# Performance work log

Measured on AMD Instinct MI355X. Metric: run time of the kernel, lower is better.

Reference implementation:

```python
import jax, jax.numpy as jnp
import numpy as np

D_MODEL = 768
NUM_HEADS = 12
HEAD_DIM = D_MODEL // NUM_HEADS
LN_EPS = 1e-5
MASK_NEG = -1000000.0


def setup_inputs() -> dict:
    key = jax.random.key(0)
    ks = jax.random.split(key, 10)
    B, L, S = 2, 2048, 2048
    s = 1.0 / np.sqrt(D_MODEL)
    return {
        "q": jax.random.normal(ks[0], (B, L, D_MODEL), jnp.float32),
        "k": jax.random.normal(ks[1], (B, S, D_MODEL), jnp.float32),
        "v": jax.random.normal(ks[2], (B, S, D_MODEL), jnp.float32),
        "attention_mask": jnp.ones((B, S), jnp.int32),
        "Wq": jax.random.normal(ks[3], (D_MODEL, D_MODEL), jnp.float32) * s,
        "Wk": jax.random.normal(ks[4], (D_MODEL, D_MODEL), jnp.float32) * s,
        "Wv": jax.random.normal(ks[5], (D_MODEL, D_MODEL), jnp.float32) * s,
        "W": jax.random.normal(ks[6], (D_MODEL, D_MODEL), jnp.float32) * s,
        "b": jnp.zeros((D_MODEL,), jnp.float32),
        "gamma": jnp.ones((D_MODEL,), jnp.float32),
        "beta": jnp.zeros((D_MODEL,), jnp.float32),
    }


def reference(q, k, v, attention_mask, Wq, Wk, Wv, W, b, gamma, beta):
    B, L, D = q.shape
    S = k.shape[1]
    H, hd = NUM_HEADS, HEAD_DIM
    # projections (torch Linear: x @ W^T), split heads -> (B,H,L,hd)
    Q = (q @ Wq.T).reshape(B, L, H, hd).transpose(0, 2, 1, 3)
    K = (k @ Wk.T).reshape(B, S, H, hd).transpose(0, 2, 1, 3)
    V = (v @ Wv.T).reshape(B, S, H, hd).transpose(0, 2, 1, 3)
    # scores (B,H,L,S) with additive key-padding mask
    scores = jnp.einsum("bhld,bhsd->bhls", Q, K) / np.sqrt(hd)
    mask_score = (1.0 - attention_mask.astype(q.dtype))[:, None, None, :] * MASK_NEG
    att = jax.nn.softmax(scores + mask_score, axis=-1)  # dropout p=0 (eval)
    # attend, merge heads, output projection (with bias)
    O = jnp.einsum("bhls,bhsd->bhld", att, V).transpose(0, 2, 1, 3).reshape(B, L, D)
    O = O @ W.T + b  # state dropout p=0 (eval)
    # residual + LayerNorm
    x = q + O
    mu = jnp.mean(x, axis=-1, keepdims=True)
    var = jnp.mean(jnp.square(x - mu), axis=-1, keepdims=True)
    return (x - mu) * jax.lax.rsqrt(var + LN_EPS) * gamma + beta
```

## Files before the change

kernel.cpp:

```cpp
#include <hip/hip_runtime.h>
#include <hip/hip_bf16.h>
#include <math.h>


typedef unsigned short u16;
typedef unsigned int   u32;
typedef __bf16 bf16x8 __attribute__((ext_vector_type(8)));
typedef float  f32x4  __attribute__((ext_vector_type(4)));

#define DM   768
#define MR   4096
#define WSZ  589824

#define LOG2E 1.44269504089f
#define SM_C  15.0f
#define K1    (0.125f * LOG2E)

__device__ inline u16 bfbits(float f) {
    union { __bf16 b; u16 u; } x; x.b = (__bf16)f; return x.u;
}

__device__ inline uint4 cvt8(const float* src) {
    const float4* p = reinterpret_cast<const float4*>(src);
    float4 a = p[0], b = p[1];
    union { __bf16 h[8]; uint4 v; } u;
    u.h[0] = (__bf16)a.x; u.h[1] = (__bf16)a.y; u.h[2] = (__bf16)a.z; u.h[3] = (__bf16)a.w;
    u.h[4] = (__bf16)b.x; u.h[5] = (__bf16)b.y; u.h[6] = (__bf16)b.z; u.h[7] = (__bf16)b.w;
    return u.v;
}

__device__ inline uint4 cvt8v(float4 a, float4 b) {
    union { __bf16 h[8]; uint4 v; } u;
    u.h[0] = (__bf16)a.x; u.h[1] = (__bf16)a.y; u.h[2] = (__bf16)a.z; u.h[3] = (__bf16)a.w;
    u.h[4] = (__bf16)b.x; u.h[5] = (__bf16)b.y; u.h[6] = (__bf16)b.z; u.h[7] = (__bf16)b.w;
    return u.v;
}

__global__ __launch_bounds__(256) void wcvt(
    const float* __restrict__ w0, const float* __restrict__ w1,
    const float* __restrict__ w2, const float* __restrict__ w3,
    u16* __restrict__ dst)
{
    const float* src = (blockIdx.y == 0) ? w0 : (blockIdx.y == 1) ? w1
                     : (blockIdx.y == 2) ? w2 : w3;
    size_t idx = ((size_t)blockIdx.x * 256 + threadIdx.x) * 8;
    *reinterpret_cast<uint4*>(&dst[(size_t)blockIdx.y * WSZ + idx]) = cvt8(&src[idx]);
}

__global__ __launch_bounds__(256, 2) void gemm_qkv(
    const float* __restrict__ xq, const float* __restrict__ xk, const float* __restrict__ xv,
    const u16* __restrict__ Wb4,
    u16* __restrict__ oq, u16* __restrict__ ok, u16* __restrict__ ov)
{
    const int mode = blockIdx.z;
    const float* X = (mode == 0) ? xq : (mode == 1) ? xk : xv;
    const u16* Wb  = Wb4 + (size_t)mode * WSZ;
    u16* out       = (mode == 0) ? oq : (mode == 1) ? ok : ov;

    __shared__ __attribute__((aligned(16))) u16 As[2][64][72];
    __shared__ __attribute__((aligned(16))) u16 Bs[64][72];

    const int tid  = threadIdx.x;
    const int lane = tid & 63;
    const int w    = tid >> 6;
    const int wm   = (w >> 1) * 32;
    const int wn   = (w & 1) * 32;
    const int quad = lane >> 4;
    const int l16  = lane & 15;
    const int tm   = blockIdx.x * 64;
    const int tn   = blockIdx.y * 64;

    const int row0 = tid >> 3,         col0 = (tid & 7) * 8;
    const int row1 = (tid + 256) >> 3, col1 = ((tid + 256) & 7) * 8;

    const float* a0p = &X[(size_t)(tm + row0) * 768 + col0];
    const float* a1p = &X[(size_t)(tm + row1) * 768 + col1];
    const u16*   b0p = &Wb[(size_t)(tn + row0) * 768 + col0];
    const u16*   b1p = &Wb[(size_t)(tn + row1) * 768 + col1];

    f32x4 acc[2][2] = {};

    *reinterpret_cast<uint4*>(&As[0][row0][col0]) = cvt8(a0p);
    *reinterpret_cast<uint4*>(&As[0][row1][col1]) = cvt8(a1p);
    uint4 bt0 = *reinterpret_cast<const uint4*>(b0p);
    uint4 bt1 = *reinterpret_cast<const uint4*>(b1p);

    for (int kt = 0; kt < 12; kt++) {
        const int cur = kt & 1;
        if (kt) __syncthreads();
        *reinterpret_cast<uint4*>(&Bs[row0][col0]) = bt0;
        *reinterpret_cast<uint4*>(&Bs[row1][col1]) = bt1;
        __syncthreads();

        float4 af0a, af0b, af1a, af1b;
        if (kt < 11) {
            const int ko = (kt + 1) * 64;
            af0a = *reinterpret_cast<const float4*>(a0p + ko);
            af0b = *reinterpret_cast<const float4*>(a0p + ko + 4);
            af1a = *reinterpret_cast<const float4*>(a1p + ko);
            af1b = *reinterpret_cast<const float4*>(a1p + ko + 4);
            bt0  = *reinterpret_cast<const uint4*>(b0p + ko);
            bt1  = *reinterpret_cast<const uint4*>(b1p + ko);
        }

        #pragma unroll
        for (int kk = 0; kk < 2; kk++) {
            bf16x8 a0 = *reinterpret_cast<const bf16x8*>(&As[cur][wm + l16     ][kk*32 + quad*8]);
            bf16x8 a1 = *reinterpret_cast<const bf16x8*>(&As[cur][wm + 16 + l16][kk*32 + quad*8]);
            bf16x8 b0 = *reinterpret_cast<const bf16x8*>(&Bs[wn + l16     ][kk*32 + quad*8]);
            bf16x8 b1 = *reinterpret_cast<const bf16x8*>(&Bs[wn + 16 + l16][kk*32 + quad*8]);
            acc[0][0] = __builtin_amdgcn_mfma_f32_16x16x32_bf16(a0, b0, acc[0][0], 0, 0, 0);
            acc[0][1] = __builtin_amdgcn_mfma_f32_16x16x32_bf16(a0, b1, acc[0][1], 0, 0, 0);
            acc[1][0] = __builtin_amdgcn_mfma_f32_16x16x32_bf16(a1, b0, acc[1][0], 0, 0, 0);
            acc[1][1] = __builtin_amdgcn_mfma_f32_16x16x32_bf16(a1, b1, acc[1][1], 0, 0, 0);
        }

        if (kt < 11) {
            const int nxt = cur ^ 1;
            *reinterpret_cast<uint4*>(&As[nxt][row0][col0]) = cvt8v(af0a, af0b);
            *reinterpret_cast<uint4*>(&As[nxt][row1][col1]) = cvt8v(af1a, af1b);
        }
    }

    #pragma unroll
    for (int i = 0; i < 2; i++)
        #pragma unroll
        for (int j = 0; j < 2; j++)
            #pragma unroll
            for (int r = 0; r < 4; r++) {
                int gm = tm + wm + i * 16 + quad * 4 + r;
                int gn = tn + wn + j * 16 + l16;
                int b = gm >> 11, l = gm & 2047;
                int h = gn >> 6,  d = gn & 63;
                u16 bv = bfbits(acc[i][j][r]);
                if (mode == 2)
                    out[((size_t)(b * 12 + h) * 64 + d) * 2048 + l] = bv;
                else
                    out[((size_t)(b * 12 + h) * 2048 + l) * 64 + d] = bv;
            }
}

__global__ __launch_bounds__(256, 2) void gemm_out(
    const u16* __restrict__ Oa, const u16* __restrict__ Wb,
    const float* __restrict__ bias, const float* __restrict__ resid,
    float* __restrict__ Xb)
{
    __shared__ __attribute__((aligned(16))) u16 As[2][64][72];
    __shared__ __attribute__((aligned(16))) u16 Bs[64][72];

    const int tid  = threadIdx.x;
    const int lane = tid & 63;
    const int w    = tid >> 6;
    const int wm   = (w >> 1) * 32;
    const int wn   = (w & 1) * 32;
    const int quad = lane >> 4;
    const int l16  = lane & 15;
    const int tm   = blockIdx.x * 64;
    const int tn   = blockIdx.y * 64;

    const int row0 = tid >> 3,         col0 = (tid & 7) * 8;
    const int row1 = (tid + 256) >> 3, col1 = ((tid + 256) & 7) * 8;

    const u16* a0p = &Oa[(size_t)(tm + row0) * 768 + col0];
    const u16* a1p = &Oa[(size_t)(tm + row1) * 768 + col1];
    const u16* b0p = &Wb[(size_t)(tn + row0) * 768 + col0];
    const u16* b1p = &Wb[(size_t)(tn + row1) * 768 + col1];

    f32x4 acc[2][2] = {};

    *reinterpret_cast<uint4*>(&As[0][row0][col0]) = *reinterpret_cast<const uint4*>(a0p);
    *reinterpret_cast<uint4*>(&As[0][row1][col1]) = *reinterpret_cast<const uint4*>(a1p);
    uint4 bt0 = *reinterpret_cast<const uint4*>(b0p);
    uint4 bt1 = *reinterpret_cast<const uint4*>(b1p);

    for (int kt = 0; kt < 12; kt++) {
        const int cur = kt & 1;
        if (kt) __syncthreads();
        *reinterpret_cast<uint4*>(&Bs[row0][col0]) = bt0;
        *reinterpret_cast<uint4*>(&Bs[row1][col1]) = bt1;
        __syncthreads();

        uint4 at0, at1;
        if (kt < 11) {
            const int ko = (kt + 1) * 64;
            at0 = *reinterpret_cast<const uint4*>(a0p + ko);
            at1 = *reinterpret_cast<const uint4*>(a1p + ko);
            bt0 = *reinterpret_cast<const uint4*>(b0p + ko);
            bt1 = *reinterpret_cast<const uint4*>(b1p + ko);
        }

        #pragma unroll
        for (int kk = 0; kk < 2; kk++) {
            bf16x8 a0 = *reinterpret_cast<const bf16x8*>(&As[cur][wm + l16     ][kk*32 + quad*8]);
            bf16x8 a1 = *reinterpret_cast<const bf16x8*>(&As[cur][wm + 16 + l16][kk*32 + quad*8]);
            bf16x8 b0 = *reinterpret_cast<const bf16x8*>(&Bs[wn + l16     ][kk*32 + quad*8]);
            bf16x8 b1 = *reinterpret_cast<const bf16x8*>(&Bs[wn + 16 + l16][kk*32 + quad*8]);
            acc[0][0] = __builtin_amdgcn_mfma_f32_16x16x32_bf16(a0, b0, acc[0][0], 0, 0, 0);
            acc[0][1] = __builtin_amdgcn_mfma_f32_16x16x32_bf16(a0, b1, acc[0][1], 0, 0, 0);
            acc[1][0] = __builtin_amdgcn_mfma_f32_16x16x32_bf16(a1, b0, acc[1][0], 0, 0, 0);
            acc[1][1] = __builtin_amdgcn_mfma_f32_16x16x32_bf16(a1, b1, acc[1][1], 0, 0, 0);
        }

        if (kt < 11) {
            const int nxt = cur ^ 1;
            *reinterpret_cast<uint4*>(&As[nxt][row0][col0]) = at0;
            *reinterpret_cast<uint4*>(&As[nxt][row1][col1]) = at1;
        }
    }

    #pragma unroll
    for (int i = 0; i < 2; i++)
        #pragma unroll
        for (int j = 0; j < 2; j++)
            #pragma unroll
            for (int r = 0; r < 4; r++) {
                int gm = tm + wm + i * 16 + quad * 4 + r;
                int gn = tn + wn + j * 16 + l16;
                Xb[(size_t)gm * 768 + gn] = acc[i][j][r] + bias[gn] + resid[(size_t)gm * 768 + gn];
            }
}

__global__ __launch_bounds__(256, 3) void attn(
    const u16* __restrict__ Qp, const u16* __restrict__ Kp, const u16* __restrict__ Vt,
    const int* __restrict__ amask, u16* __restrict__ Oatt)
{
    __shared__ __attribute__((aligned(16))) unsigned char smem[4 * 64 * 40 * 2 + 2048 * 4];
    u16 (*Ps)[64][40] = reinterpret_cast<u16(*)[64][40]>(smem);
    float* maskC = reinterpret_cast<float*>(smem + 20480);
    float (*Obuf)[68] = reinterpret_cast<float(*)[68]>(smem);

    const int tid  = threadIdx.x;
    const int lane = tid & 63;
    const int w    = tid >> 6;
    const int quad = lane >> 4;
    const int l16  = lane & 15;
    const int qt = blockIdx.x;
    const int h  = blockIdx.y;
    const int b  = blockIdx.z;

    #pragma unroll
    for (int i = 0; i < 8; i++) {
        int s = tid + i * 256;
        maskC[s] = amask[b * 2048 + s] ? (-SM_C * LOG2E) : -2.0e6f;
    }
    __syncthreads();

    const u16* Qbase = Qp + ((size_t)(b * 12 + h) * 2048 + qt * 64) * 64;
    const u16* Kb2   = Kp + (size_t)(b * 12 + h) * 2048 * 64 + (size_t)w * 32 * 64;
    const u16* Vb2   = Vt + (size_t)(b * 12 + h) * 64 * 2048 + (size_t)w * 32;

    bf16x8 qfrag[4][2];
    #pragma unroll
    for (int qb = 0; qb < 4; qb++)
        #pragma unroll
        for (int kk = 0; kk < 2; kk++)
            qfrag[qb][kk] = *reinterpret_cast<const bf16x8*>(
                &Qbase[(qb * 16 + l16) * 64 + kk * 32 + quad * 8]);

    bf16x8 onesf = {};
    if (l16 == 0) {
        #pragma unroll
        for (int i = 0; i < 8; i++) onesf[i] = (__bf16)1.0f;
    }

    f32x4 oacc[4][4] = {};
    f32x4 sacc[4]    = {};

    bf16x8 kf[2][2], vf[4];
    #pragma unroll
    for (int ct = 0; ct < 2; ct++)
        #pragma unroll
        for (int kk = 0; kk < 2; kk++)
            kf[ct][kk] = *reinterpret_cast<const bf16x8*>(
                &Kb2[(size_t)(ct * 16 + l16) * 64 + kk * 32 + quad * 8]);
    #pragma unroll
    for (int cd = 0; cd < 4; cd++)
        vf[cd] = *reinterpret_cast<const bf16x8*>(
            &Vb2[(size_t)(cd * 16 + l16) * 2048 + quad * 8]);

    for (int st = 0; st < 16; st++) {
        const int stn = (st + 1) & 15;

        #pragma unroll
        for (int ct = 0; ct < 2; ct++) {
            f32x4 sv[4];
            #pragma unroll
            for (int qb = 0; qb < 4; qb++) {
                f32x4 s = {};
                s = __builtin_amdgcn_mfma_f32_16x16x32_bf16(kf[ct][0], qfrag[qb][0], s, 0, 0, 0);
                s = __builtin_amdgcn_mfma_f32_16x16x32_bf16(kf[ct][1], qfrag[qb][1], s, 0, 0, 0);
                sv[qb] = s;
            }
            #pragma unroll
            for (int kk = 0; kk < 2; kk++)
                kf[ct][kk] = *reinterpret_cast<const bf16x8*>(
                    &Kb2[(size_t)(stn * 128 + ct * 16 + l16) * 64 + kk * 32 + quad * 8]);

            f32x4 cc = *reinterpret_cast<const f32x4*>(
                &maskC[st * 128 + w * 32 + ct * 16 + quad * 4]);
            #pragma unroll
            for (int qb = 0; qb < 4; qb++) {
                union { u16 h[4]; uint2 v2; } pk;
                #pragma unroll
                for (int r = 0; r < 4; r++)
                    pk.h[r] = bfbits(__builtin_amdgcn_exp2f(__builtin_fmaf(sv[qb][r], K1, cc[r])));
                *reinterpret_cast<uint2*>(&Ps[w][qb * 16 + l16][ct * 16 + quad * 4]) = pk.v2;
            }
        }

        bf16x8 pf[4];
        #pragma unroll
        for (int qb = 0; qb < 4; qb++)
            pf[qb] = *reinterpret_cast<const bf16x8*>(&Ps[w][qb * 16 + l16][quad * 8]);
        #pragma unroll
        for (int qb = 0; qb < 4; qb++)
            sacc[qb] = __builtin_amdgcn_mfma_f32_16x16x32_bf16(pf[qb], onesf, sacc[qb], 0, 0, 0);
        #pragma unroll
        for (int qb = 0; qb < 4; qb++)
            #pragma unroll
            for (int cd = 0; cd < 4; cd++)
                oacc[qb][cd] = __builtin_amdgcn_mfma_f32_16x16x32_bf16(pf[qb], vf[cd], oacc[qb][cd], 0, 0, 0);

        #pragma unroll
        for (int cd = 0; cd < 4; cd++)
            vf[cd] = *reinterpret_cast<const bf16x8*>(
                &Vb2[(size_t)(cd * 16 + l16) * 2048 + stn * 128 + quad * 8]);
    }

    __syncthreads();
    for (int wv = 0; wv < 4; wv++) {
        if (w == wv) {
            #pragma unroll
            for (int qb = 0; qb < 4; qb++) {
                #pragma unroll
                for (int cd = 0; cd < 4; cd++)
                    #pragma unroll
                    for (int r = 0; r < 4; r++) {
                        float* cell = &Obuf[qb * 16 + quad * 4 + r][cd * 16 + l16];
                        if (wv == 0) *cell = oacc[qb][cd][r];
                        else         *cell += oacc[qb][cd][r];
                    }
                if (l16 == 0) {
                    #pragma unroll
                    for (int r = 0; r < 4; r++) {
                        float* cell = &Obuf[qb * 16 + quad * 4 + r][64];
                        if (wv == 0) *cell = sacc[qb][r];
                        else         *cell += sacc[qb][r];
                    }
                }
            }
        }
        __syncthreads();
    }

    #pragma unroll
    for (int g = 0; g < 4; g++) {
        int unit = tid + g * 256;
        int row = unit >> 4;
        int c4  = (unit & 15) * 4;
        float rinv = 1.0f / Obuf[row][64];
        union { u16 h[4]; uint2 v; } o;
        #pragma unroll
        for (int j = 0; j < 4; j++)
            o.h[j] = bfbits(Obuf[row][c4 + j] * rinv);
        *reinterpret_cast<uint2*>(
            &Oatt[(size_t)(b * 2048 + qt * 64 + row) * 768 + h * 64 + c4]) = o.v;
    }
}

__global__ __launch_bounds__(256) void ln_kernel(
    float* __restrict__ X, const float* __restrict__ gamma,
    const float* __restrict__ beta)
{
    const int tid  = threadIdx.x;
    const int w    = tid >> 6;
    const int lane = tid & 63;
    const int row  = blockIdx.x * 4 + w;
    float* xr = X + (size_t)row * 768;

    float4 v[3];
    float s = 0.f, s2 = 0.f;
    #pragma unroll
    for (int i = 0; i < 3; i++) {
        v[i] = *reinterpret_cast<const float4*>(&xr[i * 256 + lane * 4]);
        s  += v[i].x + v[i].y + v[i].z + v[i].w;
        s2 += v[i].x * v[i].x + v[i].y * v[i].y + v[i].z * v[i].z + v[i].w * v[i].w;
    }
    #pragma unroll
    for (int off = 32; off >= 1; off >>= 1) {
        s  += __shfl_xor(s,  off, 64);
        s2 += __shfl_xor(s2, off, 64);
    }
    float mu  = s * (1.0f / 768.0f);
    float var = s2 * (1.0f / 768.0f) - mu * mu;
    float rstd = rsqrtf(var + 1e-5f);
    #pragma unroll
    for (int i = 0; i < 3; i++) {
        int c = i * 256 + lane * 4;
        float4 g  = *reinterpret_cast<const float4*>(&gamma[c]);
        float4 bt = *reinterpret_cast<const float4*>(&beta[c]);
        float4 o;
        o.x = (v[i].x - mu) * rstd * g.x + bt.x;
        o.y = (v[i].y - mu) * rstd * g.y + bt.y;
        o.z = (v[i].z - mu) * rstd * g.z + bt.z;
        o.w = (v[i].w - mu) * rstd * g.w + bt.w;
        *reinterpret_cast<float4*>(&xr[c]) = o;
    }
}

extern "C" void kernel_launch(void* const* d_in, const int* in_sizes, int n_in,
                              void* d_out, int out_size, void* d_ws, size_t ws_size,
                              hipStream_t stream)
{
    const float* q   = (const float*)d_in[0];
    const float* k   = (const float*)d_in[1];
    const float* v   = (const float*)d_in[2];
    const int*   am  = (const int*)d_in[3];
    const float* Wq  = (const float*)d_in[4];
    const float* Wk  = (const float*)d_in[5];
    const float* Wv  = (const float*)d_in[6];
    const float* W   = (const float*)d_in[7];
    const float* bb  = (const float*)d_in[8];
    const float* gam = (const float*)d_in[9];
    const float* bet = (const float*)d_in[10];

    u16* Wb4 = (u16*)d_ws;
    u16* Qp  = Wb4 + (size_t)4 * WSZ;
    u16* Kp  = Qp + (size_t)MR * DM;
    u16* Vt  = Kp + (size_t)MR * DM;
    u16* Oa  = Vt + (size_t)MR * DM;
    float* Xb = (float*)d_out;

    wcvt<<<dim3(288, 4), 256, 0, stream>>>(Wq, Wk, Wv, W, Wb4);
    gemm_qkv<<<dim3(64, 12, 3), 256, 0, stream>>>(q, k, v, Wb4, Qp, Kp, Vt);
    attn<<<dim3(32, 12, 2), 256, 0, stream>>>(Qp, Kp, Vt, am, Oa);
    gemm_out<<<dim3(64, 12), 256, 0, stream>>>(Oa, Wb4 + (size_t)3 * WSZ, bb, q, Xb);
    ln_kernel<<<1024, 256, 0, stream>>>(Xb, gam, bet);
}
```

Before: 214.9 us.

## Fuse weight bf16 conversion into GEMMs and split attention queries across 8 waves

Removes the separate weight-conversion kernel and has the QKV and output GEMMs load fp32 weights and convert them to bf16 while staging into shared memory. This saves one launch and the bf16 weight round-trip, but each GEMM block now reads twice as many weight bytes and converts the same weight tiles repeatedly. The attention kernel goes from 256 to 512 threads: 8 waves arranged as 4 key slices by 2 query halves, each holding half the accumulators. This lowers per-wave register use to raise occupancy, at the cost of every wave reading its full K/V slice, so K/V loads per block double.

```diff
diff --git a/kernel.cpp b/kernel.cpp
--- a/kernel.cpp
+++ b/kernel.cpp
@@ -10,7 +10,6 @@
 
 #define DM   768
 #define MR   4096
-#define WSZ  589824
 
 #define LOG2E 1.44269504089f
 #define SM_C  15.0f
@@ -36,26 +35,15 @@
     return u.v;
 }
 
-__global__ __launch_bounds__(256) void wcvt(
-    const float* __restrict__ w0, const float* __restrict__ w1,
-    const float* __restrict__ w2, const float* __restrict__ w3,
-    u16* __restrict__ dst)
-{
-    const float* src = (blockIdx.y == 0) ? w0 : (blockIdx.y == 1) ? w1
-                     : (blockIdx.y == 2) ? w2 : w3;
-    size_t idx = ((size_t)blockIdx.x * 256 + threadIdx.x) * 8;
-    *reinterpret_cast<uint4*>(&dst[(size_t)blockIdx.y * WSZ + idx]) = cvt8(&src[idx]);
-}
-
 __global__ __launch_bounds__(256, 2) void gemm_qkv(
     const float* __restrict__ xq, const float* __restrict__ xk, const float* __restrict__ xv,
-    const u16* __restrict__ Wb4,
+    const float* __restrict__ Wq, const float* __restrict__ Wk, const float* __restrict__ Wv,
     u16* __restrict__ oq, u16* __restrict__ ok, u16* __restrict__ ov)
 {
     const int mode = blockIdx.z;
-    const float* X = (mode == 0) ? xq : (mode == 1) ? xk : xv;
-    const u16* Wb  = Wb4 + (size_t)mode * WSZ;
-    u16* out       = (mode == 0) ? oq : (mode == 1) ? ok : ov;
+    const float* X  = (mode == 0) ? xq : (mode == 1) ? xk : xv;
+    const float* Wf = (mode == 0) ? Wq : (mode == 1) ? Wk : Wv;
+    u16* out        = (mode == 0) ? oq : (mode == 1) ? ok : ov;
 
     __shared__ __attribute__((aligned(16))) u16 As[2][64][72];
     __shared__ __attribute__((aligned(16))) u16 Bs[64][72];
@@ -75,21 +63,23 @@
 
     const float* a0p = &X[(size_t)(tm + row0) * 768 + col0];
     const float* a1p = &X[(size_t)(tm + row1) * 768 + col1];
-    const u16*   b0p = &Wb[(size_t)(tn + row0) * 768 + col0];
-    const u16*   b1p = &Wb[(size_t)(tn + row1) * 768 + col1];
+    const float* b0p = &Wf[(size_t)(tn + row0) * 768 + col0];
+    const float* b1p = &Wf[(size_t)(tn + row1) * 768 + col1];
 
     f32x4 acc[2][2] = {};
 
     *reinterpret_cast<uint4*>(&As[0][row0][col0]) = cvt8(a0p);
     *reinterpret_cast<uint4*>(&As[0][row1][col1]) = cvt8(a1p);
-    uint4 bt0 = *reinterpret_cast<const uint4*>(b0p);
-    uint4 bt1 = *reinterpret_cast<const uint4*>(b1p);
+    float4 bf0a = *reinterpret_cast<const float4*>(b0p);
+    float4 bf0b = *reinterpret_cast<const float4*>(b0p + 4);
+    float4 bf1a = *reinterpret_cast<const float4*>(b1p);
+    float4 bf1b = *reinterpret_cast<const float4*>(b1p + 4);
 
     for (int kt = 0; kt < 12; kt++) {
         const int cur = kt & 1;
         if (kt) __syncthreads();
-        *reinterpret_cast<uint4*>(&Bs[row0][col0]) = bt0;
-        *reinterpret_cast<uint4*>(&Bs[row1][col1]) = bt1;
+        *reinterpret_cast<uint4*>(&Bs[row0][col0]) = cvt8v(bf0a, bf0b);
+        *reinterpret_cast<uint4*>(&Bs[row1][col1]) = cvt8v(bf1a, bf1b);
         __syncthreads();
 
         float4 af0a, af0b, af1a, af1b;
@@ -99,8 +89,10 @@
             af0b = *reinterpret_cast<const float4*>(a0p + ko + 4);
             af1a = *reinterpret_cast<const float4*>(a1p + ko);
             af1b = *reinterpret_cast<const float4*>(a1p + ko + 4);
-            bt0  = *reinterpret_cast<const uint4*>(b0p + ko);
-            bt1  = *reinterpret_cast<const uint4*>(b1p + ko);
+            bf0a = *reinterpret_cast<const float4*>(b0p + ko);
+            bf0b = *reinterpret_cast<const float4*>(b0p + ko + 4);
+            bf1a = *reinterpret_cast<const float4*>(b1p + ko);
+            bf1b = *reinterpret_cast<const float4*>(b1p + ko + 4);
         }
 
         #pragma unroll
@@ -141,7 +133,7 @@
 }
 
 __global__ __launch_bounds__(256, 2) void gemm_out(
-    const u16* __restrict__ Oa, const u16* __restrict__ Wb,
+    const u16* __restrict__ Oa, const float* __restrict__ Wf,
     const float* __restrict__ bias, const float* __restrict__ resid,
     float* __restrict__ Xb)
 {
@@ -161,23 +153,25 @@
     const int row0 = tid >> 3,         col0 = (tid & 7) * 8;
     const int row1 = (tid + 256) >> 3, col1 = ((tid + 256) & 7) * 8;
 
-    const u16* a0p = &Oa[(size_t)(tm + row0) * 768 + col0];
-    const u16* a1p = &Oa[(size_t)(tm + row1) * 768 + col1];
-    const u16* b0p = &Wb[(size_t)(tn + row0) * 768 + col0];
-    const u16* b1p = &Wb[(size_t)(tn + row1) * 768 + col1];
+    const u16*   a0p = &Oa[(size_t)(tm + row0) * 768 + col0];
+    const u16*   a1p = &Oa[(size_t)(tm + row1) * 768 + col1];
+    const float* b0p = &Wf[(size_t)(tn + row0) * 768 + col0];
+    const float* b1p = &Wf[(size_t)(tn + row1) * 768 + col1];
 
     f32x4 acc[2][2] = {};
 
     *reinterpret_cast<uint4*>(&As[0][row0][col0]) = *reinterpret_cast<const uint4*>(a0p);
     *reinterpret_cast<uint4*>(&As[0][row1][col1]) = *reinterpret_cast<const uint4*>(a1p);
-    uint4 bt0 = *reinterpret_cast<const uint4*>(b0p);
-    uint4 bt1 = *reinterpret_cast<const uint4*>(b1p);
+    float4 bf0a = *reinterpret_cast<const float4*>(b0p);
+    float4 bf0b = *reinterpret_cast<const float4*>(b0p + 4);
+    float4 bf1a = *reinterpret_cast<const float4*>(b1p);
+    float4 bf1b = *reinterpret_cast<const float4*>(b1p + 4);
 
     for (int kt = 0; kt < 12; kt++) {
         const int cur = kt & 1;
         if (kt) __syncthreads();
-        *reinterpret_cast<uint4*>(&Bs[row0][col0]) = bt0;
-        *reinterpret_cast<uint4*>(&Bs[row1][col1]) = bt1;
+        *reinterpret_cast<uint4*>(&Bs[row0][col0]) = cvt8v(bf0a, bf0b);
+        *reinterpret_cast<uint4*>(&Bs[row1][col1]) = cvt8v(bf1a, bf1b);
         __syncthreads();
 
         uint4 at0, at1;
@@ -185,8 +179,10 @@
             const int ko = (kt + 1) * 64;
             at0 = *reinterpret_cast<const uint4*>(a0p + ko);
             at1 = *reinterpret_cast<const uint4*>(a1p + ko);
-            bt0 = *reinterpret_cast<const uint4*>(b0p + ko);
-            bt1 = *reinterpret_cast<const uint4*>(b1p + ko);
+            bf0a = *reinterpret_cast<const float4*>(b0p + ko);
+            bf0b = *reinterpret_cast<const float4*>(b0p + ko + 4);
+            bf1a = *reinterpret_cast<const float4*>(b1p + ko);
+            bf1b = *reinterpret_cast<const float4*>(b1p + ko + 4);
         }
 
         #pragma unroll
@@ -220,7 +216,7 @@
             }
 }
 
-__global__ __launch_bounds__(256, 3) void attn(
+__global__ __launch_bounds__(512, 4) void attn(
     const u16* __restrict__ Qp, const u16* __restrict__ Kp, const u16* __restrict__ Vt,
     const int* __restrict__ amask, u16* __restrict__ Oatt)
 {
@@ -232,6 +228,8 @@
     const int tid  = threadIdx.x;
     const int lane = tid & 63;
     const int w    = tid >> 6;
+    const int wk   = w & 3;
+    const int wq   = w >> 2;
     const int quad = lane >> 4;
     const int l16  = lane & 15;
     const int qt = blockIdx.x;
@@ -239,23 +237,23 @@
     const int b  = blockIdx.z;
 
     #pragma unroll
-    for (int i = 0; i < 8; i++) {
-        int s = tid + i * 256;
+    for (int i = 0; i < 4; i++) {
+        int s = tid + i * 512;
         maskC[s] = amask[b * 2048 + s] ? (-SM_C * LOG2E) : -2.0e6f;
     }
     __syncthreads();
 
     const u16* Qbase = Qp + ((size_t)(b * 12 + h) * 2048 + qt * 64) * 64;
-    const u16* Kb2   = Kp + (size_t)(b * 12 + h) * 2048 * 64 + (size_t)w * 32 * 64;
-    const u16* Vb2   = Vt + (size_t)(b * 12 + h) * 64 * 2048 + (size_t)w * 32;
-
-    bf16x8 qfrag[4][2];
-    #pragma unroll
-    for (int qb = 0; qb < 4; qb++)
+    const u16* Kb2   = Kp + (size_t)(b * 12 + h) * 2048 * 64 + (size_t)wk * 32 * 64;
+    const u16* Vb2   = Vt + (size_t)(b * 12 + h) * 64 * 2048 + (size_t)wk * 32;
+
+    bf16x8 qfrag[2][2];
+    #pragma unroll
+    for (int q = 0; q < 2; q++)
         #pragma unroll
         for (int kk = 0; kk < 2; kk++)
-            qfrag[qb][kk] = *reinterpret_cast<const bf16x8*>(
-                &Qbase[(qb * 16 + l16) * 64 + kk * 32 + quad * 8]);
+            qfrag[q][kk] = *reinterpret_cast<const bf16x8*>(
+                &Qbase[((wq * 2 + q) * 16 + l16) * 64 + kk * 32 + quad * 8]);
 
     bf16x8 onesf = {};
     if (l16 == 0) {
@@ -263,8 +261,8 @@
         for (int i = 0; i < 8; i++) onesf[i] = (__bf16)1.0f;
     }
 
-    f32x4 oacc[4][4] = {};
-    f32x4 sacc[4]    = {};
+    f32x4 oacc[2][4] = {};
+    f32x4 sacc[2]    = {};
 
     bf16x8 kf[2][2], vf[4];
     #pragma unroll
@@ -283,13 +281,13 @@
 
         #pragma unroll
         for (int ct = 0; ct < 2; ct++) {
-            f32x4 sv[4];
-            #pragma unroll
-            for (int qb = 0; qb < 4; qb++) {
+            f32x4 sv[2];
+            #pragma unroll
+            for (int q = 0; q < 2; q++) {
                 f32x4 s = {};
-                s = __builtin_amdgcn_mfma_f32_16x16x32_bf16(kf[ct][0], qfrag[qb][0], s, 0, 0, 0);
-                s = __builtin_amdgcn_mfma_f32_16x16x32_bf16(kf[ct][1], qfrag[qb][1], s, 0, 0, 0);
-                sv[qb] = s;
+                s = __builtin_amdgcn_mfma_f32_16x16x32_bf16(kf[ct][0], qfrag[q][0], s, 0, 0, 0);
+                s = __builtin_amdgcn_mfma_f32_16x16x32_bf16(kf[ct][1], qfrag[q][1], s, 0, 0, 0);
+                sv[q] = s;
             }
             #pragma unroll
             for (int kk = 0; kk < 2; kk++)
@@ -297,29 +295,31 @@
                     &Kb2[(size_t)(stn * 128 + ct * 16 + l16) * 64 + kk * 32 + quad * 8]);
 
             f32x4 cc = *reinterpret_cast<const f32x4*>(
-                &maskC[st * 128 + w * 32 + ct * 16 + quad * 4]);
-            #pragma unroll
-            for (int qb = 0; qb < 4; qb++) {
+                &maskC[st * 128 + wk * 32 + ct * 16 + quad * 4]);
+            #pragma unroll
+            for (int q = 0; q < 2; q++) {
                 union { u16 h[4]; uint2 v2; } pk;
                 #pragma unroll
                 for (int r = 0; r < 4; r++)
-                    pk.h[r] = bfbits(__builtin_amdgcn_exp2f(__builtin_fmaf(sv[qb][r], K1, cc[r])));
-                *reinterpret_cast<uint2*>(&Ps[w][qb * 16 + l16][ct * 16 + quad * 4]) = pk.v2;
+                    pk.h[r] = bfbits(__builtin_amdgcn_exp2f(__builtin_fmaf(sv[q][r], K1, cc[r])));
+                *reinterpret_cast<uint2*>(
+                    &Ps[wk][(wq * 2 + q) * 16 + l16][ct * 16 + quad * 4]) = pk.v2;
             }
         }
 
-        bf16x8 pf[4];
-        #pragma unroll
-        for (int qb = 0; qb < 4; qb++)
-            pf[qb] = *reinterpret_cast<const bf16x8*>(&Ps[w][qb * 16 + l16][quad * 8]);
-        #pragma unroll
-        for (int qb = 0; qb < 4; qb++)
-            sacc[qb] = __builtin_amdgcn_mfma_f32_16x16x32_bf16(pf[qb], onesf, sacc[qb], 0, 0, 0);
-        #pragma unroll
-        for (int qb = 0; qb < 4; qb++)
+        bf16x8 pf[2];
+        #pragma unroll
+        for (int q = 0; q < 2; q++)
+            pf[q] = *reinterpret_cast<const bf16x8*>(
+                &Ps[wk][(wq * 2 + q) * 16 + l16][quad * 8]);
+        #pragma unroll
+        for (int q = 0; q < 2; q++)
+            sacc[q] = __builtin_amdgcn_mfma_f32_16x16x32_bf16(pf[q], onesf, sacc[q], 0, 0, 0);
+        #pragma unroll
+        for (int q = 0; q < 2; q++)
             #pragma unroll
             for (int cd = 0; cd < 4; cd++)
-                oacc[qb][cd] = __builtin_amdgcn_mfma_f32_16x16x32_bf16(pf[qb], vf[cd], oacc[qb][cd], 0, 0, 0);
+                oacc[q][cd] = __builtin_amdgcn_mfma_f32_16x16x32_bf16(pf[q], vf[cd], oacc[q][cd], 0, 0, 0);
 
         #pragma unroll
         for (int cd = 0; cd < 4; cd++)
@@ -329,23 +329,24 @@
 
     __syncthreads();
     for (int wv = 0; wv < 4; wv++) {
-        if (w == wv) {
-            #pragma unroll
-            for (int qb = 0; qb < 4; qb++) {
+        if (wk == wv) {
+            #pragma unroll
+            for (int q = 0; q < 2; q++) {
+                const int rowb = (wq * 2 + q) * 16;
                 #pragma unroll
                 for (int cd = 0; cd < 4; cd++)
                     #pragma unroll
                     for (int r = 0; r < 4; r++) {
-                        float* cell = &Obuf[qb * 16 + quad * 4 + r][cd * 16 + l16];
-                        if (wv == 0) *cell = oacc[qb][cd][r];
-                        else         *cell += oacc[qb][cd][r];
+                        float* cell = &Obuf[rowb + quad * 4 + r][cd * 16 + l16];
+                        if (wv == 0) *cell = oacc[q][cd][r];
+                        else         *cell += oacc[q][cd][r];
                     }
                 if (l16 == 0) {
                     #pragma unroll
                     for (int r = 0; r < 4; r++) {
-                        float* cell = &Obuf[qb * 16 + quad * 4 + r][64];
-                        if (wv == 0) *cell = sacc[qb][r];
-                        else         *cell += sacc[qb][r];
+                        float* cell = &Obuf[rowb + quad * 4 + r][64];
+                        if (wv == 0) *cell = sacc[q][r];
+                        else         *cell += sacc[q][r];
                     }
                 }
             }
@@ -354,8 +355,8 @@
     }
 
     #pragma unroll
-    for (int g = 0; g < 4; g++) {
-        int unit = tid + g * 256;
+    for (int g = 0; g < 2; g++) {
+        int unit = tid + g * 512;
         int row = unit >> 4;
         int c4  = (unit & 15) * 4;
         float rinv = 1.0f / Obuf[row][64];
@@ -424,16 +425,14 @@
     const float* gam = (const float*)d_in[9];
     const float* bet = (const float*)d_in[10];
 
-    u16* Wb4 = (u16*)d_ws;
-    u16* Qp  = Wb4 + (size_t)4 * WSZ;
+    u16* Qp  = (u16*)d_ws;
     u16* Kp  = Qp + (size_t)MR * DM;
     u16* Vt  = Kp + (size_t)MR * DM;
     u16* Oa  = Vt + (size_t)MR * DM;
     float* Xb = (float*)d_out;
 
-    wcvt<<<dim3(288, 4), 256, 0, stream>>>(Wq, Wk, Wv, W, Wb4);
-    gemm_qkv<<<dim3(64, 12, 3), 256, 0, stream>>>(q, k, v, Wb4, Qp, Kp, Vt);
-    attn<<<dim3(32, 12, 2), 256, 0, stream>>>(Qp, Kp, Vt, am, Oa);
-    gemm_out<<<dim3(64, 12), 256, 0, stream>>>(Oa, Wb4 + (size_t)3 * WSZ, bb, q, Xb);
+    gemm_qkv<<<dim3(64, 12, 3), 256, 0, stream>>>(q, k, v, Wq, Wk, Wv, Qp, Kp, Vt);
+    attn<<<dim3(32, 12, 2), 512, 0, stream>>>(Qp, Kp, Vt, am, Oa);
+    gemm_out<<<dim3(64, 12), 256, 0, stream>>>(Oa, W, bb, q, Xb);
     ln_kernel<<<1024, 256, 0, stream>>>(Xb, gam, bet);
 }
```

New measurement: 254.8 us. 1.19x slower.

## Fuse LayerNorm into output GEMM via last-block atomic counter per row tile

Applied to the files above, without the earlier changes.

Drops the separate LayerNorm kernel. Each output-GEMM block bumps a per-row-tile atomic counter after writing its tile, and the last of the 12 column blocks for a row tile applies LayerNorm to those 64 rows. The counters are zeroed inside the attention kernel. This saves one launch and the gap between kernels, but the final block per row tile now runs the LayerNorm serially (16 iterations), which adds tail latency and needs fences for correctness.

```diff
diff --git a/kernel.cpp b/kernel.cpp
--- a/kernel.cpp
+++ b/kernel.cpp
@@ -143,10 +143,12 @@
 __global__ __launch_bounds__(256, 2) void gemm_out(
     const u16* __restrict__ Oa, const u16* __restrict__ Wb,
     const float* __restrict__ bias, const float* __restrict__ resid,
-    float* __restrict__ Xb)
+    float* __restrict__ Xb, u32* __restrict__ cnt,
+    const float* __restrict__ gamma, const float* __restrict__ beta)
 {
     __shared__ __attribute__((aligned(16))) u16 As[2][64][72];
     __shared__ __attribute__((aligned(16))) u16 Bs[64][72];
+    __shared__ int lastFlag;
 
     const int tid  = threadIdx.x;
     const int lane = tid & 63;
@@ -218,11 +220,55 @@
                 int gn = tn + wn + j * 16 + l16;
                 Xb[(size_t)gm * 768 + gn] = acc[i][j][r] + bias[gn] + resid[(size_t)gm * 768 + gn];
             }
+
+    __threadfence();
+    __syncthreads();
+    if (tid == 0) {
+        u32 old = __hip_atomic_fetch_add(&cnt[blockIdx.x], 1u,
+                                         __ATOMIC_ACQ_REL, __HIP_MEMORY_SCOPE_AGENT);
+        lastFlag = (old == 11);
+    }
+    __syncthreads();
+    if (!lastFlag) return;
+    __threadfence();
+
+    for (int it = 0; it < 16; it++) {
+        int row = tm + it * 4 + w;
+        float* xr = Xb + (size_t)row * 768;
+        float4 v[3];
+        float s = 0.f, s2 = 0.f;
+        #pragma unroll
+        for (int i = 0; i < 3; i++) {
+            v[i] = *reinterpret_cast<const float4*>(&xr[i * 256 + lane * 4]);
+            s  += v[i].x + v[i].y + v[i].z + v[i].w;
+            s2 += v[i].x * v[i].x + v[i].y * v[i].y + v[i].z * v[i].z + v[i].w * v[i].w;
+        }
+        #pragma unroll
+        for (int off = 32; off >= 1; off >>= 1) {
+            s  += __shfl_xor(s,  off, 64);
+            s2 += __shfl_xor(s2, off, 64);
+        }
+        float mu  = s * (1.0f / 768.0f);
+        float var = s2 * (1.0f / 768.0f) - mu * mu;
+        float rstd = rsqrtf(var + 1e-5f);
+        #pragma unroll
+        for (int i = 0; i < 3; i++) {
+            int c = i * 256 + lane * 4;
+            float4 g  = *reinterpret_cast<const float4*>(&gamma[c]);
+            float4 bt = *reinterpret_cast<const float4*>(&beta[c]);
+            float4 o;
+            o.x = (v[i].x - mu) * rstd * g.x + bt.x;
+            o.y = (v[i].y - mu) * rstd * g.y + bt.y;
+            o.z = (v[i].z - mu) * rstd * g.z + bt.z;
+            o.w = (v[i].w - mu) * rstd * g.w + bt.w;
+            *reinterpret_cast<float4*>(&xr[c]) = o;
+        }
+    }
 }
 
 __global__ __launch_bounds__(256, 3) void attn(
     const u16* __restrict__ Qp, const u16* __restrict__ Kp, const u16* __restrict__ Vt,
-    const int* __restrict__ amask, u16* __restrict__ Oatt)
+    const int* __restrict__ amask, u16* __restrict__ Oatt, u32* __restrict__ cnt)
 {
     __shared__ __attribute__((aligned(16))) unsigned char smem[4 * 64 * 40 * 2 + 2048 * 4];
     u16 (*Ps)[64][40] = reinterpret_cast<u16(*)[64][40]>(smem);
@@ -237,6 +283,8 @@
     const int qt = blockIdx.x;
     const int h  = blockIdx.y;
     const int b  = blockIdx.z;
+
+    if (qt == 0 && h == 0 && b == 0 && tid < 64) cnt[tid] = 0;
 
     #pragma unroll
     for (int i = 0; i < 8; i++) {
@@ -368,46 +416,6 @@
     }
 }
 
-__global__ __launch_bounds__(256) void ln_kernel(
-    float* __restrict__ X, const float* __restrict__ gamma,
-    const float* __restrict__ beta)
-{
-    const int tid  = threadIdx.x;
-    const int w    = tid >> 6;
-    const int lane = tid & 63;
-    const int row  = blockIdx.x * 4 + w;
-    float* xr = X + (size_t)row * 768;
-
-    float4 v[3];
-    float s = 0.f, s2 = 0.f;
-    #pragma unroll
-    for (int i = 0; i < 3; i++) {
-        v[i] = *reinterpret_cast<const float4*>(&xr[i * 256 + lane * 4]);
-        s  += v[i].x + v[i].y + v[i].z + v[i].w;
-        s2 += v[i].x * v[i].x + v[i].y * v[i].y + v[i].z * v[i].z + v[i].w * v[i].w;
-    }
-    #pragma unroll
-    for (int off = 32; off >= 1; off >>= 1) {
-        s  += __shfl_xor(s,  off, 64);
-        s2 += __shfl_xor(s2, off, 64);
-    }
-    float mu  = s * (1.0f / 768.0f);
-    float var = s2 * (1.0f / 768.0f) - mu * mu;
-    float rstd = rsqrtf(var + 1e-5f);
-    #pragma unroll
-    for (int i = 0; i < 3; i++) {
-        int c = i * 256 + lane * 4;
-        float4 g  = *reinterpret_cast<const float4*>(&gamma[c]);
-        float4 bt = *reinterpret_cast<const float4*>(&beta[c]);
-        float4 o;
-        o.x = (v[i].x - mu) * rstd * g.x + bt.x;
-        o.y = (v[i].y - mu) * rstd * g.y + bt.y;
-        o.z = (v[i].z - mu) * rstd * g.z + bt.z;
-        o.w = (v[i].w - mu) * rstd * g.w + bt.w;
-        *reinterpret_cast<float4*>(&xr[c]) = o;
-    }
-}
-
 extern "C" void kernel_launch(void* const* d_in, const int* in_sizes, int n_in,
                               void* d_out, int out_size, void* d_ws, size_t ws_size,
                               hipStream_t stream)
@@ -429,11 +437,12 @@
     u16* Kp  = Qp + (size_t)MR * DM;
     u16* Vt  = Kp + (size_t)MR * DM;
     u16* Oa  = Vt + (size_t)MR * DM;
+    u32* cnt = (u32*)(Oa + (size_t)MR * DM);
     float* Xb = (float*)d_out;
 
     wcvt<<<dim3(288, 4), 256, 0, stream>>>(Wq, Wk, Wv, W, Wb4);
     gemm_qkv<<<dim3(64, 12, 3), 256, 0, stream>>>(q, k, v, Wb4, Qp, Kp, Vt);
-    attn<<<dim3(32, 12, 2), 256, 0, stream>>>(Qp, Kp, Vt, am, Oa);
-    gemm_out<<<dim3(64, 12), 256, 0, stream>>>(Oa, Wb4 + (size_t)3 * WSZ, bb, q, Xb);
-    ln_kernel<<<1024, 256, 0, stream>>>(Xb, gam, bet);
-}
+    attn<<<dim3(32, 12, 2), 256, 0, stream>>>(Qp, Kp, Vt, am, Oa, cnt);
+    gemm_out<<<dim3(64, 12), 256, 0, stream>>>(Oa, Wb4 + (size_t)3 * WSZ, bb, q, Xb,
+                                               cnt, gam, bet);
+}
```

New measurement: 337.8 us. 57.2% more time.
